# Performance work log

Hardware: AMD Instinct MI355X
Metric: run time of the kernel (lower is better)

## Reference

```python
import jax, jax.numpy as jnp
import numpy as np

N_NODES = 100000
IN_F = 128
H_F = 128
LOOKBACK = 3
N_EDGES = 640000


def setup_inputs() -> dict:
    key = jax.random.key(0)
    ks = jax.random.split(key, 16)
    s = lambda k, shp: jax.random.normal(k, shp, dtype=jnp.float32) * 0.05
    inp = {
        "feat": jax.random.normal(ks[0], (N_NODES, IN_F), dtype=jnp.float32),
        "edges": jax.random.randint(ks[1], (LOOKBACK, 2, N_EDGES), 0, N_NODES, dtype=jnp.int32),
        # conv1 (SAGEConv pool, in->h) params
        "Wp1": s(ks[2], (IN_F, IN_F)), "bp1": jnp.zeros((IN_F,), jnp.float32),
        "Ws1": s(ks[3], (H_F, IN_F)), "Wn1": s(ks[4], (H_F, IN_F)), "b1": jnp.zeros((H_F,), jnp.float32),
        # BatchNorm1d affine params (training-mode batch stats)
        "gamma": jnp.ones((H_F,), jnp.float32), "beta": jnp.zeros((H_F,), jnp.float32),
        # conv2 (SAGEConv pool, h->h) params
        "Wp2": s(ks[5], (H_F, H_F)), "bp2": jnp.zeros((H_F,), jnp.float32),
        "Ws2": s(ks[6], (H_F, H_F)), "Wn2": s(ks[7], (H_F, H_F)), "b2": jnp.zeros((H_F,), jnp.float32),
    }
    return inp


def _sage_pool_conv(h, src, dst, Wp, bp, Ws, Wn, b):
    # pool aggregator: m = relu(fc_pool(h)); neigh = max over in-edges
    m = jax.nn.relu(h @ Wp.T + bp)                      # [N, d]
    agg = jax.ops.segment_max(m[src], dst, num_segments=N_NODES)  # [N, d]
    agg = jnp.where(jnp.isfinite(agg), agg, 0.0)        # nodes with no in-edges -> 0
    return h @ Ws.T + agg @ Wn.T + b


def _batchnorm(x, gamma, beta, eps=1e-5):
    mu = jnp.mean(x, axis=0)
    var = jnp.var(x, axis=0)
    return (x - mu) * jax.lax.rsqrt(var + eps) * gamma + beta


def reference(feat, edges, Wp1, bp1, Ws1, Wn1, b1, gamma, beta, Wp2, bp2, Ws2, Wn2, b2):
    def per_graph(e):
        src, dst = e[0], e[1]
        h = _sage_pool_conv(feat, src, dst, Wp1, bp1, Ws1, Wn1, b1)
        h = _batchnorm(h, gamma, beta)
        h = jax.nn.relu(h)
        h = _sage_pool_conv(h, src, dst, Wp2, bp2, Ws2, Wn2, b2)
        return h

    return jax.vmap(per_graph)(edges)  # [lookback, N, H_F]
```

## Files before the change

### kernel.cpp

```cpp
#include <hip/hip_runtime.h>
#include <hip/hip_bf16.h>

#define NNODES 100000
#define FD 128
#define NEDGES 640000
#define NB 391
#define GEMM_GRID 782
#define OFFS_U32 100032
#define BNRED 64

typedef __bf16 bf16x8 __attribute__((ext_vector_type(8)));
typedef __bf16 bf16x4 __attribute__((ext_vector_type(4)));
typedef float f32x4 __attribute__((ext_vector_type(4)));
typedef unsigned short u16x8 __attribute__((ext_vector_type(8)));

__device__ __forceinline__ bf16x8 cvt8(float4 a, float4 b) {
  bf16x8 r;
  r[0] = (__bf16)a.x; r[1] = (__bf16)a.y; r[2] = (__bf16)a.z; r[3] = (__bf16)a.w;
  r[4] = (__bf16)b.x; r[5] = (__bf16)b.y; r[6] = (__bf16)b.z; r[7] = (__bf16)b.w;
  return r;
}

__global__ __launch_bounds__(256) void packw6_k(
    const float* __restrict__ W0, const float* __restrict__ W1,
    const float* __restrict__ W2, const float* __restrict__ W3,
    const float* __restrict__ W4, const float* __restrict__ W5,
    __bf16* __restrict__ out) {
  const int gidx = blockIdx.x * 256 + threadIdx.x;
  const int wi = gidx >> 11;
  const int f = gidx & 2047;
  const float* W = wi == 0 ? W0 : wi == 1 ? W1 : wi == 2 ? W2
                 : wi == 3 ? W3 : wi == 4 ? W4 : W5;
  const int c = f >> 8, kk = (f >> 6) & 3, lane = f & 63;
  const int lr = lane & 15, lg = lane >> 4;
  const float* p = W + (c * 16 + lr) * FD + kk * 32 + lg * 8;
  *(bf16x8*)(out + (long)gidx * 8) = cvt8(*(const float4*)p, *(const float4*)(p + 4));
}

template <int AM>
__device__ __forceinline__ void load_arow(const void* __restrict__ A, long row,
                                          int kbase, const float* __restrict__ scsh,
                                          bf16x8 (&af)[4]) {
  if constexpr (AM == 1) {
#pragma unroll
    for (int kk = 0; kk < 4; ++kk)
      af[kk] = *(const bf16x8*)((const __bf16*)A + row * FD + kbase + kk * 32);
  } else if constexpr (AM == 3) {
#pragma unroll
    for (int kk = 0; kk < 4; ++kk) {
      const int k = kbase + kk * 32;
      const bf16x8 r = *(const bf16x8*)((const __bf16*)A + row * FD + k);
      const float4 scx = *(const float4*)(scsh + k);
      const float4 scy = *(const float4*)(scsh + k + 4);
      const float4 shx = *(const float4*)(scsh + 128 + k);
      const float4 shy = *(const float4*)(scsh + 128 + k + 4);
      bf16x8 o;
      o[0] = (__bf16)fmaxf((float)r[0] * scx.x + shx.x, 0.f);
      o[1] = (__bf16)fmaxf((float)r[1] * scx.y + shx.y, 0.f);
      o[2] = (__bf16)fmaxf((float)r[2] * scx.z + shx.z, 0.f);
      o[3] = (__bf16)fmaxf((float)r[3] * scx.w + shx.w, 0.f);
      o[4] = (__bf16)fmaxf((float)r[4] * scy.x + shy.x, 0.f);
      o[5] = (__bf16)fmaxf((float)r[5] * scy.y + shy.y, 0.f);
      o[6] = (__bf16)fmaxf((float)r[6] * scy.z + shy.z, 0.f);
      o[7] = (__bf16)fmaxf((float)r[7] * scy.w + shy.w, 0.f);
      af[kk] = o;
    }
  } else {
#pragma unroll
    for (int kk = 0; kk < 4; ++kk) {
      const int k = kbase + kk * 32;
      const float* ap = (const float*)A + row * FD + k;
      af[kk] = cvt8(*(const float4*)ap, *(const float4*)(ap + 4));
    }
  }
}

template <int A0M, int A1M, bool TWOA, bool RELU, bool OUTBF16, bool STATS, bool WRITEB>
__global__ __launch_bounds__(256, 2) void gemm_k(
    const void* __restrict__ A0, long a0s, const void* __restrict__ A1, long a1s,
    const __bf16* __restrict__ W0p, const __bf16* __restrict__ W1p,
    const float* __restrict__ bias, const float* __restrict__ scsh0,
    void* __restrict__ outp, long os, float* __restrict__ pblk,
    __bf16* __restrict__ bcopy, int M) {
  const int g = blockIdx.y;
  const int wid = threadIdx.x >> 6;
  const int rw = wid & 1;
  const int cw = wid >> 1;
  const int lane = threadIdx.x & 63;
  const int lr = lane & 15;
  const int lg = lane >> 4;
  const int kbase = lg * 8;
  const int rbase = blockIdx.x * 128 + rw * 64;
  __shared__ float s_red[2][4][64];

  const void* A0g = (const char*)A0 + (long)g * a0s;
  const void* A1g = (const char*)A1 + (TWOA ? (long)g * a1s : 0);
  void* outg = (char*)outp + (long)g * os;
  const float* scshg = (A0M == 3 || A1M == 3) ? scsh0 + (long)g * 256 : nullptr;

  if constexpr (!STATS) {
    if (rbase >= M) return;
  }

  bf16x8 a0[4][4];
#pragma unroll
  for (int t = 0; t < 4; ++t) {
    long row = rbase + t * 16 + lr;
    if (row > M - 1) row = M - 1;
    load_arow<A0M>(A0g, row, kbase, scshg, a0[t]);
  }
  bf16x8 a1[4][4];
  if constexpr (TWOA) {
#pragma unroll
    for (int t = 0; t < 4; ++t) {
      long row = rbase + t * 16 + lr;
      if (row > M - 1) row = M - 1;
      load_arow<A1M>(A1g, row, kbase, scshg, a1[t]);
    }
  }

  f32x4 acc[4][4];
#pragma unroll
  for (int t = 0; t < 4; ++t)
#pragma unroll
    for (int ci = 0; ci < 4; ++ci) acc[t][ci] = (f32x4){0.f, 0.f, 0.f, 0.f};

#pragma unroll
  for (int ci = 0; ci < 4; ++ci) {
    bf16x8 bw[4];
#pragma unroll
    for (int kk = 0; kk < 4; ++kk)
      bw[kk] = *(const bf16x8*)(W0p + ((long)(((cw * 4 + ci) * 4 + kk) * 64 + lane)) * 8);
#pragma unroll
    for (int t = 0; t < 4; ++t)
#pragma unroll
      for (int kk = 0; kk < 4; ++kk)
        acc[t][ci] = __builtin_amdgcn_mfma_f32_16x16x32_bf16(bw[kk], a0[t][kk], acc[t][ci], 0, 0, 0);
  }
  if constexpr (TWOA) {
#pragma unroll
    for (int ci = 0; ci < 4; ++ci) {
      bf16x8 bw[4];
#pragma unroll
      for (int kk = 0; kk < 4; ++kk)
        bw[kk] = *(const bf16x8*)(W1p + ((long)(((cw * 4 + ci) * 4 + kk) * 64 + lane)) * 8);
#pragma unroll
      for (int t = 0; t < 4; ++t)
#pragma unroll
        for (int kk = 0; kk < 4; ++kk)
          acc[t][ci] = __builtin_amdgcn_mfma_f32_16x16x32_bf16(bw[kk], a1[t][kk], acc[t][ci], 0, 0, 0);
    }
  }

  if constexpr (WRITEB) {
    if (cw == 0) {
#pragma unroll
      for (int t = 0; t < 4; ++t) {
        const int row = rbase + t * 16 + lr;
        if (row < M)
#pragma unroll
          for (int kk = 0; kk < 4; ++kk)
            *(bf16x8*)(bcopy + (long)row * FD + kbase + kk * 32) = a0[t][kk];
      }
    }
  }

  float ps[4][4], pss[4][4];
  if constexpr (STATS) {
#pragma unroll
    for (int ci = 0; ci < 4; ++ci)
#pragma unroll
      for (int j = 0; j < 4; ++j) { ps[ci][j] = 0.f; pss[ci][j] = 0.f; }
  }

#pragma unroll
  for (int t = 0; t < 4; ++t) {
    const int row = rbase + t * 16 + lr;
    const bool ok = row < M;
#pragma unroll
    for (int ci = 0; ci < 4; ++ci) {
      const int cb = cw * 64 + ci * 16 + lg * 4;
      f32x4 v = acc[t][ci];
      if (bias) {
        const float4 bv = *(const float4*)(bias + cb);
        v[0] += bv.x; v[1] += bv.y; v[2] += bv.z; v[3] += bv.w;
      }
      if constexpr (STATS) {
        if (ok) {
#pragma unroll
          for (int j = 0; j < 4; ++j) { ps[ci][j] += v[j]; pss[ci][j] += v[j] * v[j]; }
        }
      }
      if constexpr (RELU) {
#pragma unroll
        for (int j = 0; j < 4; ++j) v[j] = fmaxf(v[j], 0.f);
      }
      if (ok) {
        if constexpr (OUTBF16) {
          bf16x4 o;
          o[0] = (__bf16)v[0]; o[1] = (__bf16)v[1];
          o[2] = (__bf16)v[2]; o[3] = (__bf16)v[3];
          *(bf16x4*)((__bf16*)outg + (long)row * FD + cb) = o;
        } else {
          *(f32x4*)((float*)outg + (long)row * FD + cb) = v;
        }
      }
    }
  }

  if constexpr (STATS) {
#pragma unroll
    for (int ci = 0; ci < 4; ++ci)
#pragma unroll
      for (int j = 0; j < 4; ++j) {
        float s = ps[ci][j], q = pss[ci][j];
        s += __shfl_xor(s, 1); s += __shfl_xor(s, 2);
        s += __shfl_xor(s, 4); s += __shfl_xor(s, 8);
        q += __shfl_xor(q, 1); q += __shfl_xor(q, 2);
        q += __shfl_xor(q, 4); q += __shfl_xor(q, 8);
        if (lr == 0) {
          s_red[0][wid][ci * 16 + lg * 4 + j] = s;
          s_red[1][wid][ci * 16 + lg * 4 + j] = q;
        }
      }
    __syncthreads();
    const int tid = threadIdx.x;
    const int wh = tid >> 7, cg = tid & 127;
    const int cwi = cg >> 6, cl = cg & 63;
    float* pblkg = pblk + (long)g * ((long)GEMM_GRID * 256);
    pblkg[(long)blockIdx.x * 256 + tid] =
        s_red[wh][cwi * 2 + 0][cl] + s_red[wh][cwi * 2 + 1][cl];
  }
}

__global__ __launch_bounds__(256) void bn_red1_k(const float* __restrict__ pblk,
                                                 float* __restrict__ pblk2) {
  const int g = blockIdx.y;
  const float* p = pblk + (long)g * GEMM_GRID * 256;
  float s = 0.f;
  for (int r = blockIdx.x; r < GEMM_GRID; r += BNRED) s += p[(long)r * 256 + threadIdx.x];
  pblk2[((long)g * BNRED + blockIdx.x) * 256 + threadIdx.x] = s;
}

__global__ __launch_bounds__(256) void bn_final2_k(const float* __restrict__ pblk2,
                                                   const float* __restrict__ gamma,
                                                   const float* __restrict__ beta,
                                                   float* __restrict__ scsh3) {
  __shared__ float s_ss[128];
  const int g = blockIdx.y;
  const int tid = threadIdx.x;
  const float* p = pblk2 + (long)g * BNRED * 256;
  float s = 0.f;
#pragma unroll
  for (int r = 0; r < BNRED; ++r) s += p[r * 256 + tid];
  if (tid >= 128) s_ss[tid - 128] = s;
  __syncthreads();
  if (tid < 128) {
    const float mu = s / (float)NNODES;
    const float var = s_ss[tid] / (float)NNODES - mu * mu;
    const float sc = rsqrtf(var + 1e-5f) * gamma[tid];
    scsh3[g * 256 + tid] = sc;
    scsh3[g * 256 + 128 + tid] = beta[tid] - mu * sc;
  }
}


__global__ __launch_bounds__(256) void hist_rank3_k(const int* __restrict__ edges,
                                                    unsigned* __restrict__ deg3,
                                                    unsigned short* __restrict__ rank3) {
  const int g = blockIdx.y;
  const int e = blockIdx.x * 256 + threadIdx.x;
  if (e < NEDGES) {
    const int d = edges[(long)g * 2 * NEDGES + NEDGES + e];
    const unsigned r = atomicAdd(&deg3[(long)g * NNODES + d], 1u);
    rank3[(long)g * NEDGES + e] = (unsigned short)r;
  }
}

__global__ __launch_bounds__(256) void blocksum3_k(const unsigned* __restrict__ deg3,
                                                   unsigned* __restrict__ bsum3) {
  __shared__ unsigned s[256];
  const int g = blockIdx.y;
  const int i = blockIdx.x * 256 + threadIdx.x;
  s[threadIdx.x] = (i < NNODES) ? deg3[(long)g * NNODES + i] : 0u;
  __syncthreads();
#pragma unroll
  for (int o = 128; o > 0; o >>= 1) {
    if (threadIdx.x < o) s[threadIdx.x] += s[threadIdx.x + o];
    __syncthreads();
  }
  if (threadIdx.x == 0) bsum3[g * NB + blockIdx.x] = s[0];
}

__global__ __launch_bounds__(512) void scanb3_k(const unsigned* __restrict__ bsum3,
                                                unsigned* __restrict__ boffs3,
                                                unsigned* __restrict__ offs3) {
  __shared__ unsigned s[512];
  const int g = blockIdx.y;
  const unsigned v = (threadIdx.x < NB) ? bsum3[g * NB + threadIdx.x] : 0u;
  s[threadIdx.x] = v;
  __syncthreads();
#pragma unroll
  for (int o = 1; o < 512; o <<= 1) {
    unsigned t = (threadIdx.x >= o) ? s[threadIdx.x - o] : 0u;
    __syncthreads();
    s[threadIdx.x] += t;
    __syncthreads();
  }
  if (threadIdx.x < NB) boffs3[g * NB + threadIdx.x] = s[threadIdx.x] - v;
  if (threadIdx.x == 0) offs3[(long)g * OFFS_U32 + NNODES] = NEDGES;
}

__global__ __launch_bounds__(256) void offsets3_k(const unsigned* __restrict__ deg3,
                                                  const unsigned* __restrict__ boffs3,
                                                  unsigned* __restrict__ offs3) {
  __shared__ unsigned s[256];
  const int g = blockIdx.y;
  const int i = blockIdx.x * 256 + threadIdx.x;
  const unsigned v = (i < NNODES) ? deg3[(long)g * NNODES + i] : 0u;
  s[threadIdx.x] = v;
  __syncthreads();
#pragma unroll
  for (int o = 1; o < 256; o <<= 1) {
    unsigned t = (threadIdx.x >= o) ? s[threadIdx.x - o] : 0u;
    __syncthreads();
    s[threadIdx.x] += t;
    __syncthreads();
  }
  const unsigned excl = s[threadIdx.x] - v + boffs3[g * NB + blockIdx.x];
  if (i < NNODES) offs3[(long)g * OFFS_U32 + i] = excl;
}

__global__ __launch_bounds__(256) void scat3_k(const int* __restrict__ edges,
                                               const unsigned* __restrict__ offs3,
                                               const unsigned short* __restrict__ rank3,
                                               int* __restrict__ ssrc3) {
  const int g = blockIdx.y;
  const int e = blockIdx.x * 256 + threadIdx.x;
  if (e < NEDGES) {
    const int s = edges[(long)g * 2 * NEDGES + e];
    const int d = edges[(long)g * 2 * NEDGES + NEDGES + e];
    const unsigned p = offs3[(long)g * OFFS_U32 + d] + rank3[(long)g * NEDGES + e];
    ssrc3[(long)g * NEDGES + p] = s;
  }
}

__global__ __launch_bounds__(256) void agg_k(const unsigned short* __restrict__ m,
                                             long ms, const int* __restrict__ ssrc3,
                                             const unsigned* __restrict__ offs3,
                                             unsigned short* __restrict__ agg3) {
  const int g = blockIdx.y;
  const unsigned short* mg = m + (long)g * ms;
  const int* ssrc = ssrc3 + (long)g * NEDGES;
  const unsigned* offs = offs3 + (long)g * OFFS_U32;
  unsigned short* agg = agg3 + (long)g * NNODES * FD;

  const int gid = blockIdx.x * 256 + threadIdx.x;
  const int node = gid >> 4;
  if (node >= NNODES) return;
  const int fl = (gid & 15) * 8;
  const unsigned beg = offs[node], end = offs[node + 1];
  u16x8 acc = {0, 0, 0, 0, 0, 0, 0, 0};
  unsigned i = beg;
  for (; i + 2 <= end; i += 2) {
    const int s0 = ssrc[i];
    const int s1 = ssrc[i + 1];
    const u16x8 v0 = *(const u16x8*)(mg + (long)s0 * FD + fl);
    const u16x8 v1 = *(const u16x8*)(mg + (long)s1 * FD + fl);
#pragma unroll
    for (int j = 0; j < 8; ++j) {
      const unsigned short mx = v0[j] > v1[j] ? v0[j] : v1[j];
      acc[j] = mx > acc[j] ? mx : acc[j];
    }
  }
  if (i < end) {
    const u16x8 v = *(const u16x8*)(mg + (long)ssrc[i] * FD + fl);
#pragma unroll
    for (int j = 0; j < 8; ++j) acc[j] = v[j] > acc[j] ? v[j] : acc[j];
  }
  *(u16x8*)(agg + (long)node * FD + fl) = acc;
}

__global__ __launch_bounds__(256) void zero_k(float4* __restrict__ p, long n4) {
  const long i = (long)blockIdx.x * 256 + threadIdx.x;
  if (i < n4) p[i] = (float4){0.f, 0.f, 0.f, 0.f};
}

extern "C" void kernel_launch(void* const* d_in, const int* in_sizes, int n_in,
                              void* d_out, int out_size, void* d_ws, size_t ws_size,
                              hipStream_t stream) {
  const float* feat = (const float*)d_in[0];
  const int* edges = (const int*)d_in[1];
  const float* Wp1 = (const float*)d_in[2];
  const float* bp1 = (const float*)d_in[3];
  const float* Ws1 = (const float*)d_in[4];
  const float* Wn1 = (const float*)d_in[5];
  const float* b1 = (const float*)d_in[6];
  const float* gamma = (const float*)d_in[7];
  const float* beta = (const float*)d_in[8];
  const float* Wp2 = (const float*)d_in[9];
  const float* bp2 = (const float*)d_in[10];
  const float* Ws2 = (const float*)d_in[11];
  const float* Wn2 = (const float*)d_in[12];
  const float* b2 = (const float*)d_in[13];

  const long SZ_BF = 25600000;
  const long SZ_F32 = 51200000;

  char* w = (char*)d_ws;
  __bf16* m1 = (__bf16*)w;
  __bf16* featb = (__bf16*)(w + 25600000);
  __bf16* h1b3 = (__bf16*)(w + 51200000);
  __bf16* aggb3 = (__bf16*)(w + 128000000);
  __bf16* m2_3 = (__bf16*)(w + 204800000);
  float* pblk3 = (float*)(w + 204800000);
  float* pblk2_3 = (float*)(w + 207202304);
  __bf16* wpk = (__bf16*)(w + 281600000);
  float* scsh3 = (float*)(w + 281796608);
  unsigned* deg3 = (unsigned*)(w + 281799680);
  unsigned* offs3 = (unsigned*)(w + 282999680);
  unsigned* bsum3 = (unsigned*)(w + 284200064);
  unsigned* boffs3 = (unsigned*)(w + 284204928);
  unsigned short* rank3 = (unsigned short*)(w + 284209792);
  int* ssrc3 = (int*)(w + 288049792);

  __bf16* Wp1p = wpk;
  __bf16* Ws1p = wpk + 16384;
  __bf16* Wn1p = wpk + 2 * 16384;
  __bf16* Wp2p = wpk + 3 * 16384;
  __bf16* Ws2p = wpk + 4 * 16384;
  __bf16* Wn2p = wpk + 5 * 16384;

  const dim3 blk(256);
  const int edgeGrid = (NEDGES + 255) / 256;
  const int aggGrid = (NNODES * 16 + 255) / 256;
  const int degZeroGrid = (3 * NNODES / 4 + 255) / 256;

  packw6_k<<<48, blk, 0, stream>>>(Wp1, Ws1, Wn1, Wp2, Ws2, Wn2, wpk);

  zero_k<<<degZeroGrid, blk, 0, stream>>>((float4*)deg3, 3L * NNODES / 4);
  hist_rank3_k<<<dim3(edgeGrid, 3), blk, 0, stream>>>(edges, deg3, rank3);
  blocksum3_k<<<dim3(NB, 3), blk, 0, stream>>>(deg3, bsum3);
  scanb3_k<<<dim3(1, 3), dim3(512), 0, stream>>>(bsum3, boffs3, offs3);
  offsets3_k<<<dim3(NB, 3), blk, 0, stream>>>(deg3, boffs3, offs3);
  scat3_k<<<dim3(edgeGrid, 3), blk, 0, stream>>>(edges, offs3, rank3, ssrc3);

  gemm_k<0, 0, false, true, true, false, true><<<dim3(GEMM_GRID, 1), blk, 0, stream>>>(
      feat, 0, nullptr, 0, Wp1p, nullptr, bp1, nullptr, m1, 0, nullptr, featb, NNODES);

  agg_k<<<dim3(aggGrid, 3), blk, 0, stream>>>((const unsigned short*)m1, 0L,
                                              ssrc3, offs3, (unsigned short*)aggb3);
  gemm_k<1, 1, true, false, true, true, false><<<dim3(GEMM_GRID, 3), blk, 0, stream>>>(
      aggb3, SZ_BF, featb, 0, Wn1p, Ws1p, b1, nullptr, h1b3, SZ_BF, pblk3, nullptr, NNODES);
  bn_red1_k<<<dim3(BNRED, 3), blk, 0, stream>>>(pblk3, pblk2_3);
  bn_final2_k<<<dim3(1, 3), blk, 0, stream>>>(pblk2_3, gamma, beta, scsh3);

  gemm_k<3, 0, false, true, true, false, false><<<dim3(GEMM_GRID, 3), blk, 0, stream>>>(
      h1b3, SZ_BF, nullptr, 0, Wp2p, nullptr, bp2, scsh3, m2_3, SZ_BF, nullptr, nullptr, NNODES);
  agg_k<<<dim3(aggGrid, 3), blk, 0, stream>>>((const unsigned short*)m2_3,
                                              (long)NNODES * FD, ssrc3, offs3,
                                              (unsigned short*)aggb3);
  gemm_k<3, 1, true, false, false, false, false><<<dim3(GEMM_GRID, 3), blk, 0, stream>>>(
      h1b3, SZ_BF, aggb3, SZ_BF, Ws2p, Wn2p, b2, scsh3, d_out, SZ_F32, nullptr, nullptr, NNODES);
}
```

Before: 563.3 us.

## Stage GEMM weights and bf16 A tiles in LDS via direct global-to-LDS loads

The GEMM kernel now stages packed weights, and bf16 A rows where they apply, into shared memory using global_load_lds. Previously each wave read weights straight from global memory, and a block only shared them across its own rows. The row tile per block drops from 128 to 64, which doubles the grid and halves the accumulator registers. The cost is up to 64KB of LDS per block, which may limit occupancy, plus extra barriers between the two weight stages.

```diff
diff --git a/kernel.cpp b/kernel.cpp
--- a/kernel.cpp
+++ b/kernel.cpp
@@ -5,7 +5,7 @@
 #define FD 128
 #define NEDGES 640000
 #define NB 391
-#define GEMM_GRID 782
+#define GRID64 1563
 #define OFFS_U32 100032
 #define BNRED 64
 
@@ -19,6 +19,34 @@
   r[0] = (__bf16)a.x; r[1] = (__bf16)a.y; r[2] = (__bf16)a.z; r[3] = (__bf16)a.w;
   r[4] = (__bf16)b.x; r[5] = (__bf16)b.y; r[6] = (__bf16)b.z; r[7] = (__bf16)b.w;
   return r;
+}
+
+__device__ __forceinline__ void gl16(const void* g, void* l) {
+  __builtin_amdgcn_global_load_lds(
+      (const __attribute__((address_space(1))) unsigned int*)g,
+      (__attribute__((address_space(3))) unsigned int*)l, 16, 0, 0);
+}
+
+__device__ __forceinline__ void stage_w32(const __bf16* Wp, char* l, int tid) {
+  const int wid = tid >> 6, lane = tid & 63;
+#pragma unroll
+  for (int i = 0; i < 8; ++i) {
+    const int off = (wid * 8 + i) * 1024;
+    gl16((const char*)Wp + off + lane * 16, l + off);
+  }
+}
+
+__device__ __forceinline__ void stage_abf(const __bf16* A, long row0, int M,
+                                          char* l, int tid) {
+  const int wid = tid >> 6;
+  long row = row0 + (tid & 63);
+  if (row > M - 1) row = M - 1;
+  const char* base = (const char*)(A + row * FD);
+#pragma unroll
+  for (int i = 0; i < 4; ++i) {
+    const int s = wid * 4 + i;
+    gl16(base + s * 16, l + s * 1024);
+  }
 }
 
 __global__ __launch_bounds__(256) void packw6_k(
@@ -37,19 +65,24 @@
   *(bf16x8*)(out + (long)gidx * 8) = cvt8(*(const float4*)p, *(const float4*)(p + 4));
 }
 
+__device__ __forceinline__ void glb_arow32(const float* A, long row, int kbase,
+                                           bf16x8 (&af)[4]) {
+#pragma unroll
+  for (int kk = 0; kk < 4; ++kk) {
+    const float* ap = A + row * FD + kbase + kk * 32;
+    af[kk] = cvt8(*(const float4*)ap, *(const float4*)(ap + 4));
+  }
+}
+
 template <int AM>
-__device__ __forceinline__ void load_arow(const void* __restrict__ A, long row,
-                                          int kbase, const float* __restrict__ scsh,
-                                          bf16x8 (&af)[4]) {
-  if constexpr (AM == 1) {
-#pragma unroll
-    for (int kk = 0; kk < 4; ++kk)
-      af[kk] = *(const bf16x8*)((const __bf16*)A + row * FD + kbase + kk * 32);
-  } else if constexpr (AM == 3) {
-#pragma unroll
-    for (int kk = 0; kk < 4; ++kk) {
-      const int k = kbase + kk * 32;
-      const bf16x8 r = *(const bf16x8*)((const __bf16*)A + row * FD + k);
+__device__ __forceinline__ void lds_abf(const char* l, int rl, int lg,
+                                        const float* __restrict__ scsh,
+                                        bf16x8 (&af)[4]) {
+#pragma unroll
+  for (int kk = 0; kk < 4; ++kk) {
+    const bf16x8 r = *(const bf16x8*)(l + (kk * 4 + lg) * 1024 + rl * 16);
+    if constexpr (AM == 3) {
+      const int k = lg * 8 + kk * 32;
       const float4 scx = *(const float4*)(scsh + k);
       const float4 scy = *(const float4*)(scsh + k + 4);
       const float4 shx = *(const float4*)(scsh + 128 + k);
@@ -64,13 +97,8 @@
       o[6] = (__bf16)fmaxf((float)r[6] * scy.z + shy.z, 0.f);
       o[7] = (__bf16)fmaxf((float)r[7] * scy.w + shy.w, 0.f);
       af[kk] = o;
-    }
-  } else {
-#pragma unroll
-    for (int kk = 0; kk < 4; ++kk) {
-      const int k = kbase + kk * 32;
-      const float* ap = (const float*)A + row * FD + k;
-      af[kk] = cvt8(*(const float4*)ap, *(const float4*)(ap + 4));
+    } else {
+      af[kk] = r;
     }
   }
 }
@@ -82,46 +110,71 @@
     const float* __restrict__ bias, const float* __restrict__ scsh0,
     void* __restrict__ outp, long os, float* __restrict__ pblk,
     __bf16* __restrict__ bcopy, int M) {
-  const int g = blockIdx.y;
-  const int wid = threadIdx.x >> 6;
+  constexpr int LSZ = TWOA ? 65536 : (A0M == 0 ? 32768 : 49152);
+  __shared__ __align__(16) char lds[LSZ];
+  char* lW0 = lds;
+  char* lA0 = lds + 32768;
+  char* lA1 = lds + 49152;
+  char* lW1 = lds + 32768;
+
+  const int g = blockIdx.y;
+  const int tid = threadIdx.x;
+  const int wid = tid >> 6;
+  const int lane = tid & 63;
   const int rw = wid & 1;
   const int cw = wid >> 1;
-  const int lane = threadIdx.x & 63;
   const int lr = lane & 15;
   const int lg = lane >> 4;
-  const int kbase = lg * 8;
-  const int rbase = blockIdx.x * 128 + rw * 64;
-  __shared__ float s_red[2][4][64];
+  const long row0 = (long)blockIdx.x * 64;
 
   const void* A0g = (const char*)A0 + (long)g * a0s;
   const void* A1g = (const char*)A1 + (TWOA ? (long)g * a1s : 0);
   void* outg = (char*)outp + (long)g * os;
   const float* scshg = (A0M == 3 || A1M == 3) ? scsh0 + (long)g * 256 : nullptr;
 
-  if constexpr (!STATS) {
-    if (rbase >= M) return;
-  }
-
-  bf16x8 a0[4][4];
-#pragma unroll
-  for (int t = 0; t < 4; ++t) {
-    long row = rbase + t * 16 + lr;
-    if (row > M - 1) row = M - 1;
-    load_arow<A0M>(A0g, row, kbase, scshg, a0[t]);
-  }
-  bf16x8 a1[4][4];
+  stage_w32(W0p, lW0, tid);
+  if constexpr (A0M != 0) stage_abf((const __bf16*)A0g, row0, M, lA0, tid);
+  if constexpr (TWOA) stage_abf((const __bf16*)A1g, row0, M, lA1, tid);
+  __syncthreads();
+
+  bf16x8 a0[2][4];
+  bf16x8 a1[2][4];
+  if constexpr (A0M == 0) {
+#pragma unroll
+    for (int t = 0; t < 2; ++t) {
+      long row = row0 + rw * 32 + t * 16 + lr;
+      if (row > M - 1) row = M - 1;
+      glb_arow32((const float*)A0g, row, lg * 8, a0[t]);
+    }
+  } else {
+#pragma unroll
+    for (int t = 0; t < 2; ++t)
+      lds_abf<A0M>(lA0, rw * 32 + t * 16 + lr, lg, scshg, a0[t]);
+  }
   if constexpr (TWOA) {
 #pragma unroll
-    for (int t = 0; t < 4; ++t) {
-      long row = rbase + t * 16 + lr;
-      if (row > M - 1) row = M - 1;
-      load_arow<A1M>(A1g, row, kbase, scshg, a1[t]);
+    for (int t = 0; t < 2; ++t)
+      lds_abf<A1M>(lA1, rw * 32 + t * 16 + lr, lg, scshg, a1[t]);
+    __syncthreads();
+    stage_w32(W1p, lW1, tid);
+  }
+
+  if constexpr (WRITEB) {
+    if (cw == 0) {
+#pragma unroll
+      for (int t = 0; t < 2; ++t) {
+        const long row = row0 + rw * 32 + t * 16 + lr;
+        if (row < M)
+#pragma unroll
+          for (int kk = 0; kk < 4; ++kk)
+            *(bf16x8*)(bcopy + row * FD + lg * 8 + kk * 32) = a0[t][kk];
+      }
     }
   }
 
-  f32x4 acc[4][4];
-#pragma unroll
-  for (int t = 0; t < 4; ++t)
+  f32x4 acc[2][4];
+#pragma unroll
+  for (int t = 0; t < 2; ++t)
 #pragma unroll
     for (int ci = 0; ci < 4; ++ci) acc[t][ci] = (f32x4){0.f, 0.f, 0.f, 0.f};
 
@@ -130,41 +183,29 @@
     bf16x8 bw[4];
 #pragma unroll
     for (int kk = 0; kk < 4; ++kk)
-      bw[kk] = *(const bf16x8*)(W0p + ((long)(((cw * 4 + ci) * 4 + kk) * 64 + lane)) * 8);
-#pragma unroll
-    for (int t = 0; t < 4; ++t)
+      bw[kk] = *(const bf16x8*)(lW0 + ((cw * 4 + ci) * 4 + kk) * 1024 + lane * 16);
+#pragma unroll
+    for (int t = 0; t < 2; ++t)
 #pragma unroll
       for (int kk = 0; kk < 4; ++kk)
         acc[t][ci] = __builtin_amdgcn_mfma_f32_16x16x32_bf16(bw[kk], a0[t][kk], acc[t][ci], 0, 0, 0);
   }
   if constexpr (TWOA) {
+    __syncthreads();
 #pragma unroll
     for (int ci = 0; ci < 4; ++ci) {
       bf16x8 bw[4];
 #pragma unroll
       for (int kk = 0; kk < 4; ++kk)
-        bw[kk] = *(const bf16x8*)(W1p + ((long)(((cw * 4 + ci) * 4 + kk) * 64 + lane)) * 8);
-#pragma unroll
-      for (int t = 0; t < 4; ++t)
+        bw[kk] = *(const bf16x8*)(lW1 + ((cw * 4 + ci) * 4 + kk) * 1024 + lane * 16);
+#pragma unroll
+      for (int t = 0; t < 2; ++t)
 #pragma unroll
         for (int kk = 0; kk < 4; ++kk)
           acc[t][ci] = __builtin_amdgcn_mfma_f32_16x16x32_bf16(bw[kk], a1[t][kk], acc[t][ci], 0, 0, 0);
     }
   }
 
-  if constexpr (WRITEB) {
-    if (cw == 0) {
-#pragma unroll
-      for (int t = 0; t < 4; ++t) {
-        const int row = rbase + t * 16 + lr;
-        if (row < M)
-#pragma unroll
-          for (int kk = 0; kk < 4; ++kk)
-            *(bf16x8*)(bcopy + (long)row * FD + kbase + kk * 32) = a0[t][kk];
-      }
-    }
-  }
-
   float ps[4][4], pss[4][4];
   if constexpr (STATS) {
 #pragma unroll
@@ -174,8 +215,8 @@
   }
 
 #pragma unroll
-  for (int t = 0; t < 4; ++t) {
-    const int row = rbase + t * 16 + lr;
+  for (int t = 0; t < 2; ++t) {
+    const long row = row0 + rw * 32 + t * 16 + lr;
     const bool ok = row < M;
 #pragma unroll
     for (int ci = 0; ci < 4; ++ci) {
@@ -200,15 +241,16 @@
           bf16x4 o;
           o[0] = (__bf16)v[0]; o[1] = (__bf16)v[1];
           o[2] = (__bf16)v[2]; o[3] = (__bf16)v[3];
-          *(bf16x4*)((__bf16*)outg + (long)row * FD + cb) = o;
+          *(bf16x4*)((__bf16*)outg + row * FD + cb) = o;
         } else {
-          *(f32x4*)((float*)outg + (long)row * FD + cb) = v;
+          *(f32x4*)((float*)outg + row * FD + cb) = v;
         }
       }
     }
   }
 
   if constexpr (STATS) {
+    __shared__ float s_red[2][4][64];
 #pragma unroll
     for (int ci = 0; ci < 4; ++ci)
 #pragma unroll
@@ -224,10 +266,9 @@
         }
       }
     __syncthreads();
-    const int tid = threadIdx.x;
     const int wh = tid >> 7, cg = tid & 127;
     const int cwi = cg >> 6, cl = cg & 63;
-    float* pblkg = pblk + (long)g * ((long)GEMM_GRID * 256);
+    float* pblkg = pblk + (long)g * ((long)GRID64 * 256);
     pblkg[(long)blockIdx.x * 256 + tid] =
         s_red[wh][cwi * 2 + 0][cl] + s_red[wh][cwi * 2 + 1][cl];
   }
@@ -236,9 +277,9 @@
 __global__ __launch_bounds__(256) void bn_red1_k(const float* __restrict__ pblk,
                                                  float* __restrict__ pblk2) {
   const int g = blockIdx.y;
-  const float* p = pblk + (long)g * GEMM_GRID * 256;
+  const float* p = pblk + (long)g * GRID64 * 256;
   float s = 0.f;
-  for (int r = blockIdx.x; r < GEMM_GRID; r += BNRED) s += p[(long)r * 256 + threadIdx.x];
+  for (int r = blockIdx.x; r < GRID64; r += BNRED) s += p[(long)r * 256 + threadIdx.x];
   pblk2[((long)g * BNRED + blockIdx.x) * 256 + threadIdx.x] = s;
 }
 
@@ -414,7 +455,7 @@
   __bf16* aggb3 = (__bf16*)(w + 128000000);
   __bf16* m2_3 = (__bf16*)(w + 204800000);
   float* pblk3 = (float*)(w + 204800000);
-  float* pblk2_3 = (float*)(w + 207202304);
+  float* pblk2_3 = (float*)(w + 209700096);
   __bf16* wpk = (__bf16*)(w + 281600000);
   float* scsh3 = (float*)(w + 281796608);
   unsigned* deg3 = (unsigned*)(w + 281799680);
@@ -445,21 +486,21 @@
   offsets3_k<<<dim3(NB, 3), blk, 0, stream>>>(deg3, boffs3, offs3);
   scat3_k<<<dim3(edgeGrid, 3), blk, 0, stream>>>(edges, offs3, rank3, ssrc3);
 
-  gemm_k<0, 0, false, true, true, false, true><<<dim3(GEMM_GRID, 1), blk, 0, stream>>>(
+  gemm_k<0, 0, false, true, true, false, true><<<dim3(GRID64, 1), blk, 0, stream>>>(
       feat, 0, nullptr, 0, Wp1p, nullptr, bp1, nullptr, m1, 0, nullptr, featb, NNODES);
 
   agg_k<<<dim3(aggGrid, 3), blk, 0, stream>>>((const unsigned short*)m1, 0L,
                                               ssrc3, offs3, (unsigned short*)aggb3);
-  gemm_k<1, 1, true, false, true, true, false><<<dim3(GEMM_GRID, 3), blk, 0, stream>>>(
+  gemm_k<1, 1, true, false, true, true, false><<<dim3(GRID64, 3), blk, 0, stream>>>(
       aggb3, SZ_BF, featb, 0, Wn1p, Ws1p, b1, nullptr, h1b3, SZ_BF, pblk3, nullptr, NNODES);
   bn_red1_k<<<dim3(BNRED, 3), blk, 0, stream>>>(pblk3, pblk2_3);
   bn_final2_k<<<dim3(1, 3), blk, 0, stream>>>(pblk2_3, gamma, beta, scsh3);
 
-  gemm_k<3, 0, false, true, true, false, false><<<dim3(GEMM_GRID, 3), blk, 0, stream>>>(
+  gemm_k<3, 0, false, true, true, false, false><<<dim3(GRID64, 3), blk, 0, stream>>>(
       h1b3, SZ_BF, nullptr, 0, Wp2p, nullptr, bp2, scsh3, m2_3, SZ_BF, nullptr, nullptr, NNODES);
   agg_k<<<dim3(aggGrid, 3), blk, 0, stream>>>((const unsigned short*)m2_3,
                                               (long)NNODES * FD, ssrc3, offs3,
                                               (unsigned short*)aggb3);
-  gemm_k<3, 1, true, false, false, false, false><<<dim3(GEMM_GRID, 3), blk, 0, stream>>>(
+  gemm_k<3, 1, true, false, false, false, false><<<dim3(GRID64, 3), blk, 0, stream>>>(
       h1b3, SZ_BF, aggb3, SZ_BF, Ws2p, Wn2p, b2, scsh3, d_out, SZ_F32, nullptr, nullptr, NNODES);
 }
```

After: 556.9 us. Within noise of the previous version (-1.1%).
